# Kernel optimization log

Hardware: AMD Instinct MI355X
Metric: run time of the kernel (lower is better)

Reference implementation:

```python
import jax, jax.numpy as jnp
import numpy as np

HEAD_DIM = 64
SCALE = 1.0 / np.sqrt(HEAD_DIM).astype(np.float32)
EPS = 1e-6


def setup_inputs() -> dict:
    key = jax.random.key(0)
    kq, kk, kv = jax.random.split(key, 3)
    shape = (2, 16, 2048, HEAD_DIM)  # [B, H, S, D]
    return {
        "q": jax.random.normal(kq, shape, dtype=jnp.float32),
        "k": jax.random.normal(kk, shape, dtype=jnp.float32),
        "v": jax.random.normal(kv, shape, dtype=jnp.float32),
    }


def reference(q, k, v):
    # scores: [B, H, S, S]
    scores = jnp.einsum("bhqd,bhkd->bhqk", q, k) * SCALE
    num = scores * scores  # p = 2 power normalization
    den = num.sum(axis=-1, keepdims=True) + EPS
    prob = num / den
    out = jnp.einsum("bhqk,bhkd->bhqd", prob, v)
    return (out, prob)
```

## Files before the change

kernel.cpp:

```cpp
#include <hip/hip_runtime.h>
#include <stdint.h>

#define S_LEN 2048
#define D_DIM 64
#define NBH   32
#define TQ    128
#define KT    64
#define NT    (S_LEN / KT)
#define SCALE_F 0.125f
#define EPS_F   1e-6f
#define SPSTR 40

typedef unsigned short us;
typedef __attribute__((ext_vector_type(8))) short bf8_t;
typedef __attribute__((ext_vector_type(4))) float f4_t;
typedef __attribute__((ext_vector_type(16))) float f16_t;
typedef __attribute__((ext_vector_type(4))) unsigned int u4_t;

#define MFMA16(a,b,c) __builtin_amdgcn_mfma_f32_16x16x32_bf16((a),(b),(c),0,0,0)
#define MFMA32(a,b,c) __builtin_amdgcn_mfma_f32_32x32x16_bf16((a),(b),(c),0,0,0)

__device__ __forceinline__ unsigned int cvtpk(float lo, float hi) {
  unsigned int d;
  asm("v_cvt_pk_bf16_f32 %0, %1, %2" : "=v"(d) : "v"(lo), "v"(hi));
  return d;
}

union u4bf8 { u4_t u; bf8_t b; };

__global__ __launch_bounds__(256) void g_kernel(const float* __restrict__ kp,
                                                float* __restrict__ g) {
  __shared__ __align__(16) float sk[64][68];
  const int bh = blockIdx.x >> 4, rc = blockIdx.x & 15;
  const int t = threadIdx.x;
  const int ti = t & 15, tj = t >> 4;
  float acc[4][4];
#pragma unroll
  for (int a = 0; a < 4; ++a)
#pragma unroll
    for (int b = 0; b < 4; ++b) acc[a][b] = 0.f;
  const float* kb = kp + ((size_t)bh * S_LEN + rc * 128) * D_DIM;
  for (int sub = 0; sub < 2; ++sub) {
    __syncthreads();
    {
      const int r = t >> 2, c0 = (t & 3) * 16;
      const float4* p = (const float4*)(kb + (size_t)(sub * 64 + r) * D_DIM + c0);
      float4 x0 = p[0], x1 = p[1], x2 = p[2], x3 = p[3];
      *(float4*)&sk[r][c0]      = x0;
      *(float4*)&sk[r][c0 + 4]  = x1;
      *(float4*)&sk[r][c0 + 8]  = x2;
      *(float4*)&sk[r][c0 + 12] = x3;
    }
    __syncthreads();
#pragma unroll 4
    for (int r = 0; r < 64; ++r) {
      float4 qi = *(const float4*)&sk[r][ti * 4];
      float4 qj = *(const float4*)&sk[r][tj * 4];
      float iv[4] = {qi.x, qi.y, qi.z, qi.w};
      float jv[4] = {qj.x, qj.y, qj.z, qj.w};
#pragma unroll
      for (int a = 0; a < 4; ++a)
#pragma unroll
        for (int b = 0; b < 4; ++b) acc[a][b] += iv[a] * jv[b];
    }
  }
  float* gb = g + ((size_t)bh << 12);
#pragma unroll
  for (int a = 0; a < 4; ++a)
#pragma unroll
    for (int b = 0; b < 4; ++b)
      atomicAdd(&gb[(ti * 4 + a) * 64 + tj * 4 + b], acc[a][b]);
}

__device__ __forceinline__ bf8_t frag_swz(const us* sp, int row, int cb) {
  return *(const bf8_t*)(sp + row * 64 + ((cb ^ (row & 7)) << 3));
}

__global__ __launch_bounds__(512, 4) void attn_main(const float* __restrict__ q,
                                                    const float* __restrict__ k,
                                                    const float* __restrict__ v,
                                                    const float* __restrict__ g,
                                                    float* __restrict__ outp,
                                                    float* __restrict__ probp) {
  __shared__ __align__(16) unsigned char smem[53248];
  us* sK  = (us*)smem;
  us* sVt = (us*)(smem + 16384);
  us* sP  = (us*)(smem + 32768);
  float* sInv = (float*)(smem + 32768);
  float* sRed = (float*)smem;

  const int lin = blockIdx.x;
  const int virt = (lin & 7) * 64 + (lin >> 3);
  const int bh = virt >> 4, qb = virt & 15;
  const int q0 = qb * TQ;
  const int t = threadIdx.x, lane = t & 63, w = t >> 6;
  const int l31 = lane & 31, hi = lane >> 5;
  const int wq = w & 3, kh = w >> 2;

  const float* kbh = k + (size_t)bh * S_LEN * D_DIM;
  const float* vbh = v + (size_t)bh * S_LEN * D_DIM;
  const float* qbh = q + (size_t)bh * S_LEN * D_DIM;

  const int kr = t >> 3, kc = t & 7;
  const int vr = (t & 31) * 2, vc = (t >> 5) * 4;

  float4 pk0, pk1, pva, pvb;
  {
    const float4* kp_ = (const float4*)(kbh + (size_t)kr * D_DIM + kc * 8);
    pk0 = kp_[0]; pk1 = kp_[1];
    const float4* vp0 = (const float4*)(vbh + (size_t)vr * D_DIM + vc);
    const float4* vp1 = (const float4*)(vbh + (size_t)(vr + 1) * D_DIM + vc);
    pva = vp0[0]; pvb = vp1[0];
  }

  bf8_t qA[4];
  {
    const float* qrow = qbh + (size_t)(q0 + wq * 32 + l31) * D_DIM;
#pragma unroll
    for (int s = 0; s < 4; ++s) {
      const float4* qp = (const float4*)(qrow + s * 16 + hi * 8);
      float4 a = qp[0], b = qp[1];
      u4bf8 x;
      x.u[0] = cvtpk(a.x * SCALE_F, a.y * SCALE_F);
      x.u[1] = cvtpk(a.z * SCALE_F, a.w * SCALE_F);
      x.u[2] = cvtpk(b.x * SCALE_F, b.y * SCALE_F);
      x.u[3] = cvtpk(b.z * SCALE_F, b.w * SCALE_F);
      qA[s] = x.b;
    }
  }

  {
    const float4* gp = (const float4*)(g + ((size_t)bh << 12) + (size_t)kr * D_DIM + kc * 8);
    float4 a = gp[0], b = gp[1];
    u4bf8 x;
    x.u[0] = cvtpk(a.x, a.y); x.u[1] = cvtpk(a.z, a.w);
    x.u[2] = cvtpk(b.x, b.y); x.u[3] = cvtpk(b.z, b.w);
    *(u4_t*)(sK + kr * 64 + ((kc ^ (kr & 7)) << 3)) = x.u;
  }
  __syncthreads();

  {
    const int lr = lane & 15, lh = lane >> 4;
    bf8_t qD[2];
    {
      const float* qbase = qbh + (size_t)(q0 + w * 16 + lr) * D_DIM;
#pragma unroll
      for (int h2 = 0; h2 < 2; ++h2) {
        const float4* qp = (const float4*)(qbase + h2 * 32 + lh * 8);
        float4 a = qp[0], b = qp[1];
        u4bf8 x;
        x.u[0] = cvtpk(a.x * SCALE_F, a.y * SCALE_F);
        x.u[1] = cvtpk(a.z * SCALE_F, a.w * SCALE_F);
        x.u[2] = cvtpk(b.x * SCALE_F, b.y * SCALE_F);
        x.u[3] = cvtpk(b.z * SCALE_F, b.w * SCALE_F);
        qD[h2] = x.b;
      }
    }
    float den[4] = {0.f, 0.f, 0.f, 0.f};
#pragma unroll
    for (int ct = 0; ct < 4; ++ct) {
      f4_t accT = {0.f, 0.f, 0.f, 0.f};
      bf8_t b0 = frag_swz(sK, ct * 16 + lr, lh);
      bf8_t b1 = frag_swz(sK, ct * 16 + lr, 4 + lh);
      accT = MFMA16(qD[0], b0, accT);
      accT = MFMA16(qD[1], b1, accT);
#pragma unroll
      for (int i = 0; i < 4; ++i) {
        float qv = qbh[(size_t)(q0 + w * 16 + lh * 4 + i) * D_DIM + ct * 16 + lr] * SCALE_F;
        den[i] += accT[i] * qv;
      }
    }
#pragma unroll
    for (int i = 0; i < 4; ++i) {
      den[i] += __shfl_xor(den[i], 1, 64);
      den[i] += __shfl_xor(den[i], 2, 64);
      den[i] += __shfl_xor(den[i], 4, 64);
      den[i] += __shfl_xor(den[i], 8, 64);
      sInv[w * 16 + lh * 4 + i] = 1.f / (den[i] + EPS_F);
    }
  }
  __syncthreads();

  float invv[16];
#pragma unroll
  for (int r = 0; r < 16; ++r)
    invv[r] = sInv[wq * 32 + (r & 3) + 8 * (r >> 2) + 4 * hi];
  __syncthreads();

  {
    u4bf8 x;
    x.u[0] = cvtpk(pk0.x, pk0.y); x.u[1] = cvtpk(pk0.z, pk0.w);
    x.u[2] = cvtpk(pk1.x, pk1.y); x.u[3] = cvtpk(pk1.z, pk1.w);
    *(u4_t*)(sK + kr * 64 + ((kc ^ (kr & 7)) << 3)) = x.u;
    unsigned int w0 = cvtpk(pva.x, pvb.x), w1 = cvtpk(pva.y, pvb.y);
    unsigned int w2 = cvtpk(pva.z, pvb.z), w3 = cvtpk(pva.w, pvb.w);
    const int cks = vr >> 3, sub = vr & 7;
    *(unsigned int*)(sVt + (vc + 0) * 64 + ((cks ^ ((vc + 0) & 7)) << 3) + sub) = w0;
    *(unsigned int*)(sVt + (vc + 1) * 64 + ((cks ^ ((vc + 1) & 7)) << 3) + sub) = w1;
    *(unsigned int*)(sVt + (vc + 2) * 64 + ((cks ^ ((vc + 2) & 7)) << 3) + sub) = w2;
    *(unsigned int*)(sVt + (vc + 3) * 64 + ((cks ^ ((vc + 3) & 7)) << 3) + sub) = w3;
  }
  __syncthreads();

  f16_t oaccA, oaccB;
#pragma unroll
  for (int i = 0; i < 16; ++i) { oaccA[i] = 0.f; oaccB[i] = 0.f; }

  us* sPw = sP + w * (32 * SPSTR);
  float* probw = probp + ((size_t)bh * S_LEN + q0 + wq * 32) * S_LEN + kh * 32 + l31;

  for (int kt = 0; kt < NT; ++kt) {
    const int cur = kt & 1, nxt = cur ^ 1;
    const us* sKc = sK + cur * 4096;
    const us* sVc = sVt + cur * 4096;
    us* sKn = sK + nxt * 4096;
    us* sVn = sVt + nxt * 4096;
    const int k0 = kt * KT;

    if (kt + 1 < NT) {
      const int k0n = k0 + KT;
      const float4* kp_ = (const float4*)(kbh + (size_t)(k0n + kr) * D_DIM + kc * 8);
      pk0 = kp_[0]; pk1 = kp_[1];
      const float4* vp0 = (const float4*)(vbh + (size_t)(k0n + vr) * D_DIM + vc);
      const float4* vp1 = (const float4*)(vbh + (size_t)(k0n + vr + 1) * D_DIM + vc);
      pva = vp0[0]; pvb = vp1[0];
    }

    f16_t cacc;
#pragma unroll
    for (int i = 0; i < 16; ++i) cacc[i] = 0.f;
#pragma unroll
    for (int s = 0; s < 4; ++s) {
      bf8_t bk = frag_swz(sKc, kh * 32 + l31, 2 * s + hi);
      cacc = MFMA32(qA[s], bk, cacc);
    }

#pragma unroll
    for (int a = 0; a < 4; ++a) {
      float p0 = cacc[4 * a + 0] * cacc[4 * a + 0] * invv[4 * a + 0];
      float p1 = cacc[4 * a + 1] * cacc[4 * a + 1] * invv[4 * a + 1];
      float p2 = cacc[4 * a + 2] * cacc[4 * a + 2] * invv[4 * a + 2];
      float p3 = cacc[4 * a + 3] * cacc[4 * a + 3] * invv[4 * a + 3];
      const int qq = 8 * a + 4 * hi;
      __builtin_nontemporal_store(p0, probw + (size_t)(qq + 0) * S_LEN + k0);
      __builtin_nontemporal_store(p1, probw + (size_t)(qq + 1) * S_LEN + k0);
      __builtin_nontemporal_store(p2, probw + (size_t)(qq + 2) * S_LEN + k0);
      __builtin_nontemporal_store(p3, probw + (size_t)(qq + 3) * S_LEN + k0);
      unsigned int c01 = cvtpk(p0, p1);
      unsigned int c23 = cvtpk(p2, p3);
      sPw[(qq + 0) * SPSTR + l31] = (us)(c01 & 0xffffu);
      sPw[(qq + 1) * SPSTR + l31] = (us)(c01 >> 16);
      sPw[(qq + 2) * SPSTR + l31] = (us)(c23 & 0xffffu);
      sPw[(qq + 3) * SPSTR + l31] = (us)(c23 >> 16);
    }

    bf8_t pa0 = *(const bf8_t*)(sPw + l31 * SPSTR + 0 * 16 + hi * 8);
    bf8_t pa1 = *(const bf8_t*)(sPw + l31 * SPSTR + 1 * 16 + hi * 8);

    bf8_t vb00 = frag_swz(sVc, 0 * 32 + l31, kh * 4 + 2 * 0 + hi);
    bf8_t vb01 = frag_swz(sVc, 1 * 32 + l31, kh * 4 + 2 * 0 + hi);
    bf8_t vb10 = frag_swz(sVc, 0 * 32 + l31, kh * 4 + 2 * 1 + hi);
    bf8_t vb11 = frag_swz(sVc, 1 * 32 + l31, kh * 4 + 2 * 1 + hi);

    oaccA = MFMA32(pa0, vb00, oaccA);
    oaccB = MFMA32(pa0, vb01, oaccB);
    oaccA = MFMA32(pa1, vb10, oaccA);
    oaccB = MFMA32(pa1, vb11, oaccB);

    if (kt + 1 < NT) {
      u4bf8 x;
      x.u[0] = cvtpk(pk0.x, pk0.y); x.u[1] = cvtpk(pk0.z, pk0.w);
      x.u[2] = cvtpk(pk1.x, pk1.y); x.u[3] = cvtpk(pk1.z, pk1.w);
      *(u4_t*)(sKn + kr * 64 + ((kc ^ (kr & 7)) << 3)) = x.u;
      unsigned int w0 = cvtpk(pva.x, pvb.x), w1 = cvtpk(pva.y, pvb.y);
      unsigned int w2 = cvtpk(pva.z, pvb.z), w3 = cvtpk(pva.w, pvb.w);
      const int cks = vr >> 3, sub = vr & 7;
      *(unsigned int*)(sVn + (vc + 0) * 64 + ((cks ^ ((vc + 0) & 7)) << 3) + sub) = w0;
      *(unsigned int*)(sVn + (vc + 1) * 64 + ((cks ^ ((vc + 1) & 7)) << 3) + sub) = w1;
      *(unsigned int*)(sVn + (vc + 2) * 64 + ((cks ^ ((vc + 2) & 7)) << 3) + sub) = w2;
      *(unsigned int*)(sVn + (vc + 3) * 64 + ((cks ^ ((vc + 3) & 7)) << 3) + sub) = w3;
    }
    __syncthreads();
  }

  if (kh == 1) {
    float* dst = sRed + wq * 2048;
#pragma unroll
    for (int i = 0; i < 4; ++i) {
      f4_t ga = {oaccA[4 * i], oaccA[4 * i + 1], oaccA[4 * i + 2], oaccA[4 * i + 3]};
      f4_t gb = {oaccB[4 * i], oaccB[4 * i + 1], oaccB[4 * i + 2], oaccB[4 * i + 3]};
      *(f4_t*)(dst + 0 * 1024 + i * 256 + lane * 4) = ga;
      *(f4_t*)(dst + 1 * 1024 + i * 256 + lane * 4) = gb;
    }
  }
  __syncthreads();
  if (kh == 0) {
    const float* src = sRed + wq * 2048;
    float* ob = outp + ((size_t)bh * S_LEN + q0 + wq * 32) * D_DIM + l31;
#pragma unroll
    for (int i = 0; i < 4; ++i) {
      f4_t ga = *(const f4_t*)(src + 0 * 1024 + i * 256 + lane * 4);
      f4_t gb = *(const f4_t*)(src + 1 * 1024 + i * 256 + lane * 4);
#pragma unroll
      for (int b = 0; b < 4; ++b) {
        const int r = 4 * i + b;
        const int qr = (r & 3) + 8 * (r >> 2) + 4 * hi;
        __builtin_nontemporal_store(oaccA[r] + ga[b], ob + (size_t)qr * D_DIM + 0);
        __builtin_nontemporal_store(oaccB[r] + gb[b], ob + (size_t)qr * D_DIM + 32);
      }
    }
  }
}

extern "C" void kernel_launch(void* const* d_in, const int* in_sizes, int n_in,
                              void* d_out, int out_size, void* d_ws, size_t ws_size,
                              hipStream_t stream) {
  (void)in_sizes; (void)n_in; (void)out_size; (void)ws_size;
  const float* q = (const float*)d_in[0];
  const float* k = (const float*)d_in[1];
  const float* v = (const float*)d_in[2];
  float* outp  = (float*)d_out;
  float* probp = outp + (size_t)NBH * S_LEN * D_DIM;
  float* g = (float*)d_ws;

  hipMemsetAsync(g, 0, (size_t)NBH * 64 * 64 * sizeof(float), stream);
  g_kernel<<<dim3(NBH * 16), dim3(256), 0, stream>>>(k, g);
  attn_main<<<dim3(512), dim3(512), 0, stream>>>(q, k, v, g, outp, probp);
}
```

Before: 164.4 us.

## Replace atomic Gram accumulation with partial buffers; hoist V loads, add MFMA priority

The K^T K Gram kernel now writes four per-chunk partial sums with plain vector stores instead of atomically adding into a zeroed buffer. The memset is removed and the main kernel sums the four partials when it loads G. The main loop also loads the V fragments earlier and wraps the MFMA sections in s_setprio. These aim to cut atomic traffic, a launch and LDS latency, but the Gram kernel now runs only 128 blocks and the workspace grows fourfold.

```diff
diff --git a/kernel.cpp b/kernel.cpp
--- a/kernel.cpp
+++ b/kernel.cpp
@@ -7,6 +7,7 @@
 #define TQ    128
 #define KT    64
 #define NT    (S_LEN / KT)
+#define RC_G  4
 #define SCALE_F 0.125f
 #define EPS_F   1e-6f
 #define SPSTR 40
@@ -29,18 +30,18 @@
 union u4bf8 { u4_t u; bf8_t b; };
 
 __global__ __launch_bounds__(256) void g_kernel(const float* __restrict__ kp,
-                                                float* __restrict__ g) {
+                                                float* __restrict__ gpart) {
   __shared__ __align__(16) float sk[64][68];
-  const int bh = blockIdx.x >> 4, rc = blockIdx.x & 15;
+  const int bh = blockIdx.x >> 2, rc = blockIdx.x & 3;
   const int t = threadIdx.x;
-  const int ti = t & 15, tj = t >> 4;
+  const int ti = t >> 4, tj = t & 15;
   float acc[4][4];
 #pragma unroll
   for (int a = 0; a < 4; ++a)
 #pragma unroll
     for (int b = 0; b < 4; ++b) acc[a][b] = 0.f;
-  const float* kb = kp + ((size_t)bh * S_LEN + rc * 128) * D_DIM;
-  for (int sub = 0; sub < 2; ++sub) {
+  const float* kb = kp + ((size_t)bh * S_LEN + rc * 512) * D_DIM;
+  for (int sub = 0; sub < 8; ++sub) {
     __syncthreads();
     {
       const int r = t >> 2, c0 = (t & 3) * 16;
@@ -64,12 +65,12 @@
         for (int b = 0; b < 4; ++b) acc[a][b] += iv[a] * jv[b];
     }
   }
-  float* gb = g + ((size_t)bh << 12);
-#pragma unroll
-  for (int a = 0; a < 4; ++a)
-#pragma unroll
-    for (int b = 0; b < 4; ++b)
-      atomicAdd(&gb[(ti * 4 + a) * 64 + tj * 4 + b], acc[a][b]);
+  float* gb = gpart + ((size_t)(rc * NBH + bh) << 12);
+#pragma unroll
+  for (int a = 0; a < 4; ++a) {
+    f4_t vv = {acc[a][0], acc[a][1], acc[a][2], acc[a][3]};
+    *(f4_t*)(gb + (ti * 4 + a) * 64 + tj * 4) = vv;
+  }
 }
 
 __device__ __forceinline__ bf8_t frag_swz(const us* sp, int row, int cb) {
@@ -79,7 +80,7 @@
 __global__ __launch_bounds__(512, 4) void attn_main(const float* __restrict__ q,
                                                     const float* __restrict__ k,
                                                     const float* __restrict__ v,
-                                                    const float* __restrict__ g,
+                                                    const float* __restrict__ gpart,
                                                     float* __restrict__ outp,
                                                     float* __restrict__ probp) {
   __shared__ __align__(16) unsigned char smem[53248];
@@ -130,8 +131,16 @@
   }
 
   {
-    const float4* gp = (const float4*)(g + ((size_t)bh << 12) + (size_t)kr * D_DIM + kc * 8);
-    float4 a = gp[0], b = gp[1];
+    const float* gp = gpart + ((size_t)bh << 12) + (size_t)kr * D_DIM + kc * 8;
+    const size_t gstride = (size_t)NBH << 12;
+    float4 a = {0.f, 0.f, 0.f, 0.f}, b = {0.f, 0.f, 0.f, 0.f};
+#pragma unroll
+    for (int rc = 0; rc < RC_G; ++rc) {
+      const float4* p = (const float4*)(gp + rc * gstride);
+      float4 x = p[0], y = p[1];
+      a.x += x.x; a.y += x.y; a.z += x.z; a.w += x.w;
+      b.x += y.x; b.y += y.y; b.z += y.z; b.w += y.w;
+    }
     u4bf8 x;
     x.u[0] = cvtpk(a.x, a.y); x.u[1] = cvtpk(a.z, a.w);
     x.u[2] = cvtpk(b.x, b.y); x.u[3] = cvtpk(b.z, b.w);
@@ -226,14 +235,21 @@
       pva = vp0[0]; pvb = vp1[0];
     }
 
+    bf8_t vb00 = frag_swz(sVc, 0 * 32 + l31, kh * 4 + 2 * 0 + hi);
+    bf8_t vb01 = frag_swz(sVc, 1 * 32 + l31, kh * 4 + 2 * 0 + hi);
+    bf8_t vb10 = frag_swz(sVc, 0 * 32 + l31, kh * 4 + 2 * 1 + hi);
+    bf8_t vb11 = frag_swz(sVc, 1 * 32 + l31, kh * 4 + 2 * 1 + hi);
+
     f16_t cacc;
 #pragma unroll
     for (int i = 0; i < 16; ++i) cacc[i] = 0.f;
+    __builtin_amdgcn_s_setprio(1);
 #pragma unroll
     for (int s = 0; s < 4; ++s) {
       bf8_t bk = frag_swz(sKc, kh * 32 + l31, 2 * s + hi);
       cacc = MFMA32(qA[s], bk, cacc);
     }
+    __builtin_amdgcn_s_setprio(0);
 
 #pragma unroll
     for (int a = 0; a < 4; ++a) {
@@ -257,15 +273,12 @@
     bf8_t pa0 = *(const bf8_t*)(sPw + l31 * SPSTR + 0 * 16 + hi * 8);
     bf8_t pa1 = *(const bf8_t*)(sPw + l31 * SPSTR + 1 * 16 + hi * 8);
 
-    bf8_t vb00 = frag_swz(sVc, 0 * 32 + l31, kh * 4 + 2 * 0 + hi);
-    bf8_t vb01 = frag_swz(sVc, 1 * 32 + l31, kh * 4 + 2 * 0 + hi);
-    bf8_t vb10 = frag_swz(sVc, 0 * 32 + l31, kh * 4 + 2 * 1 + hi);
-    bf8_t vb11 = frag_swz(sVc, 1 * 32 + l31, kh * 4 + 2 * 1 + hi);
-
+    __builtin_amdgcn_s_setprio(1);
     oaccA = MFMA32(pa0, vb00, oaccA);
     oaccB = MFMA32(pa0, vb01, oaccB);
     oaccA = MFMA32(pa1, vb10, oaccA);
     oaccB = MFMA32(pa1, vb11, oaccB);
+    __builtin_amdgcn_s_setprio(0);
 
     if (kt + 1 < NT) {
       u4bf8 x;
@@ -321,9 +334,8 @@
   const float* v = (const float*)d_in[2];
   float* outp  = (float*)d_out;
   float* probp = outp + (size_t)NBH * S_LEN * D_DIM;
-  float* g = (float*)d_ws;
-
-  hipMemsetAsync(g, 0, (size_t)NBH * 64 * 64 * sizeof(float), stream);
-  g_kernel<<<dim3(NBH * 16), dim3(256), 0, stream>>>(k, g);
-  attn_main<<<dim3(512), dim3(512), 0, stream>>>(q, k, v, g, outp, probp);
-}
+  float* gpart = (float*)d_ws;
+
+  g_kernel<<<dim3(NBH * RC_G), dim3(256), 0, stream>>>(k, gpart);
+  attn_main<<<dim3(512), dim3(512), 0, stream>>>(q, k, v, gpart, outp, probp);
+}
```

Result: slower. 201.4 us (+22.5%).
